# Kernel optimization log

Measured on AMD Instinct MI355X. Metric: run time of the kernel, lower is better.

Reference implementation:

```python
import jax, jax.numpy as jnp
import numpy as np

D_MODEL, KAN_HIDDEN, NUM, K = 1024, 128, 3, 3  # grid_size=3, spline order k=3
GRID_RANGE = (-1.0, 1.0)


def make_grid(in_dim):
    # extended grid: num+1 interior knots padded by k steps of h on each side -> num+1+2k points
    h = (GRID_RANGE[1] - GRID_RANGE[0]) / NUM
    g = jnp.arange(-K, NUM + K + 1, dtype=jnp.float32) * h + GRID_RANGE[0]  # [num+1+2k]
    return jnp.broadcast_to(g, (in_dim, g.shape[0]))  # [in_dim, G]


def b_splines(x, grid):
    # Cox-de-Boor recursion. x: [N, D], grid: [D, G] -> basis [N, D, G-1-K]
    xg = x[:, :, None]  # [N, D, 1]
    B = ((xg >= grid[None, :, :-1]) & (xg < grid[None, :, 1:])).astype(x.dtype)
    for d in range(1, K + 1):
        left = (xg - grid[None, :, : -(d + 1)]) / (grid[:, d:-1] - grid[:, : -(d + 1)])[None]
        right = (grid[None, :, d + 1:] - xg) / (grid[:, d + 1:] - grid[:, 1:-d])[None]
        B = left * B[:, :, :-1] + right * B[:, :, 1:]
    return B  # [N, D, NUM+K]


def kan_layer(x, grid, coef, scale_base, scale_sp):
    # y[n,i,o] = scale_base[i,o]*silu(x[n,i]) + scale_sp[i,o]*sum_g B[n,i,g]*coef[i,o,g]; out = y.sum(i)
    B = b_splines(x, grid)  # [N, in, NUM+K]
    spline = jnp.einsum('nig,iog->no', B, coef * scale_sp[:, :, None])
    base = jnp.einsum('ni,io->no', jax.nn.silu(x), scale_base)
    return base + spline  # [N, out]


def setup_inputs() -> dict:
    key = jax.random.key(0)
    ks = jax.random.split(key, 7)
    s = 0.1  # small init scale for spline coefficients, matching noisy init spirit
    return {
        'x': jax.random.normal(ks[0], (4, 4096, D_MODEL), dtype=jnp.float32),
        'coef1': jax.random.normal(ks[1], (D_MODEL, KAN_HIDDEN, NUM + K), dtype=jnp.float32) * s,
        'scale_base1': jax.random.normal(ks[2], (D_MODEL, KAN_HIDDEN), dtype=jnp.float32),
        'scale_sp1': jnp.ones((D_MODEL, KAN_HIDDEN), dtype=jnp.float32),
        'coef2': jax.random.normal(ks[3], (KAN_HIDDEN, D_MODEL, NUM + K), dtype=jnp.float32) * s,
        'scale_base2': jax.random.normal(ks[4], (KAN_HIDDEN, D_MODEL), dtype=jnp.float32),
        'scale_sp2': jnp.ones((KAN_HIDDEN, D_MODEL), dtype=jnp.float32),
    }


def reference(x, coef1, scale_base1, scale_sp1, coef2, scale_base2, scale_sp2):
    b, s, d = x.shape
    xf = x.reshape(-1, d)  # [N, d_model]
    g1 = make_grid(D_MODEL)
    g2 = make_grid(KAN_HIDDEN)
    y1 = kan_layer(xf, g1, coef1, scale_base1, scale_sp1)   # [N, kan_hidden]
    y2 = kan_layer(y1, g2, coef2, scale_base2, scale_sp2)   # [N, d_model]
    return y2.reshape(b, s, d)
```

## Files before the change

kernel.cpp:

```cpp
#include <hip/hip_runtime.h>
#include <stdint.h>

typedef float f32x4 __attribute__((ext_vector_type(4)));
typedef __bf16 bf16x8 __attribute__((ext_vector_type(8)));
typedef __bf16 bf16x2 __attribute__((ext_vector_type(2)));
typedef unsigned short ushort4v __attribute__((ext_vector_type(4)));

#define NROW 16384
#define DM   1024
#define HID  128
#define K1   8192
#define K2   1024
#define KSPLIT 4

__device__ __forceinline__ unsigned short f2bf(float f) {
  unsigned u = __builtin_bit_cast(unsigned, f);
  u += 0x7fffu + ((u >> 16) & 1u);
  return (unsigned short)(u >> 16);
}

__device__ __forceinline__ uint32_t pk2(float lo, float hi) {
  bf16x2 v;
  v[0] = (__bf16)lo;
  v[1] = (__bf16)hi;
  return __builtin_bit_cast(uint32_t, v);
}

__device__ __forceinline__ void g2l16(const void* g, void* l) {
  __builtin_amdgcn_global_load_lds(
      (const __attribute__((address_space(1))) unsigned int*)g,
      (__attribute__((address_space(3))) unsigned int*)l, 16, 0, 0);
}

__device__ __forceinline__ bf16x8 expand8(float v) {
  const float t = (v + 3.0f) * 1.5f;
  const float cf = floorf(t);
  const float u = t - cf;
  int c = (int)cf;
  c = c < -1 ? -1 : c;
  c = c > 9 ? 9 : c;
  const float u2 = u * u, u3 = u2 * u, omu = 1.0f - u;
  const float p0 = u3 * (1.0f / 6.0f);
  float p1 = __builtin_fmaf(0.5f, u, 1.0f / 6.0f);
  p1 = __builtin_fmaf(0.5f, u2, p1);
  p1 = __builtin_fmaf(-0.5f, u3, p1);
  float p2 = __builtin_fmaf(0.5f, u3, 4.0f / 6.0f);
  p2 = p2 - u2;
  const float p3 = (omu * omu) * (omu * (1.0f / 6.0f));
  const uint64_t W = (uint64_t)pk2(p3, p2) | ((uint64_t)pk2(p1, p0) << 32);
  const int sa = (c - 2) * 16;
  const int sl = sa & 63;
  const uint64_t t1 = W << sl;
  const uint64_t t2 = (W >> (63 - sl)) >> 1;
  const uint64_t t3 = W >> ((-sa) & 63);
  const uint64_t L = sa < 0 ? t3 : (sa < 64 ? t1 : 0);
  const uint64_t H = sa < 0 ? 0  : (sa < 64 ? t2 : t1);
  const float e = __expf(-v);
  const float s = v * __builtin_amdgcn_rcpf(1.0f + e);
  const uint32_t su = __builtin_bit_cast(uint32_t, s);
  const uint32_t shf_bits = su & 0xffff0000u;
  const float slo_f = s - __builtin_bit_cast(float, shf_bits);
  const uint32_t slo = (uint32_t)__builtin_bit_cast(unsigned short, (__bf16)slo_f);
  const uint32_t w0 = ((uint32_t)L & 0xffff0000u) | (shf_bits >> 16);
  const uint32_t w1 = (uint32_t)(L >> 32);
  const uint32_t w2 = (uint32_t)H;
  const uint32_t w3 = ((uint32_t)(H >> 32) & 0xffffu) | (slo << 16);
  union { uint4 q; bf16x8 b; } r;
  r.q = (uint4){w0, w1, w2, w3};
  return r.b;
}

__global__ void kan_prep_w1(const float* __restrict__ c1, const float* __restrict__ sb1,
                            const float* __restrict__ sp1, unsigned short* __restrict__ w1t) {
  const int t = blockIdx.x * 256 + threadIdx.x;
  const int o = t >> 10, i = t & 1023;
  const float sb = sb1[i * HID + o], sp = sp1[i * HID + o];
  const float* cf = c1 + (size_t)(i * HID + o) * 6;
  union { uint4 u; unsigned short h[8]; } r;
  const unsigned short b = f2bf(sb);
  r.h[0] = b; r.h[7] = b;
#pragma unroll
  for (int g = 0; g < 6; ++g) r.h[g + 1] = f2bf(cf[g] * sp);
  *(uint4*)(w1t + (size_t)o * K1 + i * 8) = r.u;
}

__global__ void kan_prep_w2(const float* __restrict__ c2, const float* __restrict__ sb2,
                            const float* __restrict__ sp2, unsigned short* __restrict__ w2t) {
  const int t = blockIdx.x * 256 + threadIdx.x;
  const int o = t >> 7, i = t & 127;
  const float sb = sb2[i * DM + o], sp = sp2[i * DM + o];
  const float* cf = c2 + (size_t)(i * DM + o) * 6;
  union { uint4 u; unsigned short h[8]; } r;
  const unsigned short b = f2bf(sb);
  r.h[0] = b; r.h[7] = b;
#pragma unroll
  for (int g = 0; g < 6; ++g) r.h[g + 1] = f2bf(cf[g] * sp);
  *(uint4*)(w2t + (size_t)o * K2 + i * 8) = r.u;
}

__global__ __launch_bounds__(256, 2) void kan_gemm1(
    const float* __restrict__ x, const unsigned short* __restrict__ w1t,
    unsigned short* __restrict__ yq) {
  __shared__ __align__(16) char lds[65536];
  const int tid = threadIdx.x;
  const int lane = tid & 63, w = tid >> 6;
  const int wm = w >> 1, wk = w & 1;
  const int mt = blockIdx.x >> 2, kh = blockIdx.x & 3;
  const int m0 = mt * 128;

  f32x4 acc[4][8];
#pragma unroll
  for (int a = 0; a < 4; ++a)
#pragma unroll
    for (int b = 0; b < 8; ++b) acc[a][b] = (f32x4){0.f, 0.f, 0.f, 0.f};

  const int arow = m0 + wm * 64 + (lane & 15);
  const float* xp[4];
#pragma unroll
  for (int mi = 0; mi < 4; ++mi)
    xp[mi] = x + (size_t)(arow + mi * 16) * DM + kh * 256 + wk * 4 + (lane >> 4);

  const unsigned short* bp =
      w1t + (size_t)(lane & 15) * K1 + kh * 2048 + wk * 32 + (lane >> 4) * 8;

  const int NT = 32;
  float xc[4], xn[4];
#pragma unroll
  for (int mi = 0; mi < 4; ++mi) xc[mi] = xp[mi][0];

  for (int kt = 0; kt < NT; ++kt) {
    bf16x8 b[8], af[4];
#pragma unroll
    for (int ni = 0; ni < 8; ++ni)
      b[ni] = *(const bf16x8*)(bp + (size_t)ni * 16 * K1 + kt * 64);
    const int nk = (kt + 1 < NT) ? kt + 1 : NT - 1;
#pragma unroll
    for (int mi = 0; mi < 4; ++mi) xn[mi] = xp[mi][nk * 8];
#pragma unroll
    for (int mi = 0; mi < 4; ++mi) af[mi] = expand8(xc[mi]);
#pragma unroll
    for (int mi = 0; mi < 4; ++mi)
#pragma unroll
      for (int ni = 0; ni < 8; ++ni)
        acc[mi][ni] = __builtin_amdgcn_mfma_f32_16x16x32_bf16(af[mi], b[ni], acc[mi][ni], 0, 0, 0);
#pragma unroll
    for (int mi = 0; mi < 4; ++mi) xc[mi] = xn[mi];
  }

  if (wk == 1) {
    char* r = lds + wm * 32768;
#pragma unroll
    for (int mi = 0; mi < 4; ++mi)
#pragma unroll
      for (int ni = 0; ni < 8; ++ni)
        *(f32x4*)(r + (mi * 8 + ni) * 1024 + lane * 16) = acc[mi][ni];
  }
  __syncthreads();
  if (wk == 0) {
    const char* r = lds + wm * 32768;
    unsigned short* yb = yq + (size_t)kh * NROW * HID;
#pragma unroll
    for (int mi = 0; mi < 4; ++mi)
#pragma unroll
      for (int ni = 0; ni < 8; ++ni) {
        f32x4 o = *(const f32x4*)(r + (mi * 8 + ni) * 1024 + lane * 16);
        o += acc[mi][ni];
        const int col = ni * 16 + (lane & 15);
#pragma unroll
        for (int rr = 0; rr < 4; ++rr) {
          const int row = wm * 64 + mi * 16 + (lane >> 4) * 4 + rr;
          yb[(size_t)(m0 + row) * HID + col] = __builtin_bit_cast(unsigned short, (__bf16)o[rr]);
        }
      }
  }
}

__global__ void kan_combine(const unsigned short* __restrict__ yq, unsigned short* __restrict__ a2) {
  const size_t i4 = ((size_t)blockIdx.x * 256 + threadIdx.x) * 4;
  float v[4] = {0.f, 0.f, 0.f, 0.f};
#pragma unroll
  for (int h = 0; h < KSPLIT; ++h) {
    ushort4v q = *(const ushort4v*)(yq + (size_t)h * NROW * HID + i4);
#pragma unroll
    for (int j = 0; j < 4; ++j)
      v[j] += __builtin_bit_cast(float, (uint32_t)q[j] << 16);
  }
#pragma unroll
  for (int j = 0; j < 4; ++j)
    *(bf16x8*)(a2 + (i4 + j) * 8) = expand8(v[j]);
}

__global__ __launch_bounds__(256, 2) void kan_gemm2(
    const unsigned short* __restrict__ a2, const unsigned short* __restrict__ w2t,
    float* __restrict__ out) {
  __shared__ __align__(16) unsigned short lds[2 * 16384];
  const int tid = threadIdx.x;
  const int lane = tid & 63, w = tid >> 6;
  const int wm = w >> 1, wn = w & 1;
  const int mt = blockIdx.x & 127, nt = blockIdx.x >> 7;
  const int m0 = mt * 128, n0 = nt * 128;

  f32x4 acc[4][4];
#pragma unroll
  for (int a = 0; a < 4; ++a)
#pragma unroll
    for (int b = 0; b < 4; ++b) acc[a][b] = (f32x4){0.f, 0.f, 0.f, 0.f};

  auto stage = [&](int kt, int buf) {
#pragma unroll
    for (int q = 0; q < 4; ++q) {
      const int r = (w * 4 + q) * 8 + (lane >> 3);
      const int slot = (lane & 7) ^ (lane >> 3);
      g2l16(a2 + (size_t)(m0 + r) * K2 + kt * 64 + slot * 8,
            (char*)lds + buf * 32768 + (w * 4 + q) * 1024);
      g2l16(w2t + (size_t)(n0 + r) * K2 + kt * 64 + slot * 8,
            (char*)lds + buf * 32768 + 16384 + (w * 4 + q) * 1024);
    }
  };

  stage(0, 0);
  for (int kt = 0; kt < 16; ++kt) {
    const int cur = kt & 1;
    if (kt + 1 < 16) {
      stage(kt + 1, cur ^ 1);
      asm volatile("s_waitcnt vmcnt(8)" ::: "memory");
    } else {
      asm volatile("s_waitcnt vmcnt(0)" ::: "memory");
    }
    __builtin_amdgcn_sched_barrier(0);
    __builtin_amdgcn_s_barrier();
    const char* ab = (const char*)lds + cur * 32768;
    const char* bb = ab + 16384;
#pragma unroll
    for (int ks = 0; ks < 2; ++ks) {
      bf16x8 af[4], bfr[4];
#pragma unroll
      for (int mi = 0; mi < 4; ++mi) {
        const int row = wm * 64 + mi * 16 + (lane & 15);
        af[mi] = *(const bf16x8*)(ab + ((row * 128 + ks * 64 + (lane >> 4) * 16) ^ ((row & 7) << 4)));
      }
#pragma unroll
      for (int ni = 0; ni < 4; ++ni) {
        const int col = wn * 64 + ni * 16 + (lane & 15);
        bfr[ni] = *(const bf16x8*)(bb + ((col * 128 + ks * 64 + (lane >> 4) * 16) ^ ((col & 7) << 4)));
      }
#pragma unroll
      for (int mi = 0; mi < 4; ++mi)
#pragma unroll
        for (int ni = 0; ni < 4; ++ni)
          acc[mi][ni] = __builtin_amdgcn_mfma_f32_16x16x32_bf16(af[mi], bfr[ni], acc[mi][ni], 0, 0, 0);
    }
    __builtin_amdgcn_s_barrier();
  }

#pragma unroll
  for (int mi = 0; mi < 4; ++mi)
#pragma unroll
    for (int r = 0; r < 4; ++r) {
      const int row = wm * 64 + mi * 16 + (lane >> 4) * 4 + r;
#pragma unroll
      for (int ni = 0; ni < 4; ++ni) {
        const int col = wn * 64 + ni * 16 + (lane & 15);
        out[(size_t)(m0 + row) * DM + n0 + col] = acc[mi][ni][r];
      }
    }
}

extern "C" void kernel_launch(void* const* d_in, const int* in_sizes, int n_in,
                              void* d_out, int out_size, void* d_ws, size_t ws_size,
                              hipStream_t stream) {
  const float* x   = (const float*)d_in[0];
  const float* c1  = (const float*)d_in[1];
  const float* sb1 = (const float*)d_in[2];
  const float* sp1 = (const float*)d_in[3];
  const float* c2  = (const float*)d_in[4];
  const float* sb2 = (const float*)d_in[5];
  const float* sp2 = (const float*)d_in[6];
  float* out = (float*)d_out;

  unsigned short* w1t = (unsigned short*)d_ws;
  unsigned short* w2t = w1t + (size_t)HID * K1;
  unsigned short* a2  = w2t + (size_t)DM * K2;
  unsigned short* yq  = a2 + (size_t)NROW * K2;

  kan_prep_w1<<<512, 256, 0, stream>>>(c1, sb1, sp1, w1t);
  kan_prep_w2<<<512, 256, 0, stream>>>(c2, sb2, sp2, w2t);
  kan_gemm1<<<512, 256, 0, stream>>>(x, w1t, yq);
  kan_combine<<<NROW * HID / 1024, 256, 0, stream>>>(yq, a2);
  kan_gemm2<<<(NROW / 128) * (DM / 128), 256, 0, stream>>>(a2, w2t, out);
}
```

Before: 157.5 us.

## Pre-swizzle layer-1 weights into MFMA fragment order and vectorize x loads

The layer-1 weight prep kernel now writes bf16 weights in a packed layout that matches the MFMA fragment order per wave, so each lane's B loads are contiguous across the wave instead of strided by K1 rows. The k-assignment of x is changed so each lane reads four consecutive floats with one 16-byte load per four k-steps, rather than one scalar load per step. This targets uncoalesced global loads in gemm1. It also changes which input features each wave and lane cover, which must stay consistent with the new weight layout.

```diff
diff --git a/kernel.cpp b/kernel.cpp
--- a/kernel.cpp
+++ b/kernel.cpp
@@ -71,7 +71,7 @@
 }
 
 __global__ void kan_prep_w1(const float* __restrict__ c1, const float* __restrict__ sb1,
-                            const float* __restrict__ sp1, unsigned short* __restrict__ w1t) {
+                            const float* __restrict__ sp1, unsigned short* __restrict__ w1p) {
   const int t = blockIdx.x * 256 + threadIdx.x;
   const int o = t >> 10, i = t & 1023;
   const float sb = sb1[i * HID + o], sp = sp1[i * HID + o];
@@ -81,7 +81,11 @@
   r.h[0] = b; r.h[7] = b;
 #pragma unroll
   for (int g = 0; g < 6; ++g) r.h[g + 1] = f2bf(cf[g] * sp);
-  *(uint4*)(w1t + (size_t)o * K1 + i * 8) = r.u;
+  const int kh = i >> 8, iq = i & 255;
+  const int wk = iq >> 7, gg = (iq >> 5) & 3, it = iq & 31;
+  const int lane = gg * 16 + (o & 15), ni = o >> 4;
+  const size_t flat = (size_t)kh * 262144 + it * 8192 + wk * 4096 + ni * 512 + lane * 8;
+  *(uint4*)(w1p + flat) = r.u;
 }
 
 __global__ void kan_prep_w2(const float* __restrict__ c2, const float* __restrict__ sb2,
@@ -99,7 +103,7 @@
 }
 
 __global__ __launch_bounds__(256, 2) void kan_gemm1(
-    const float* __restrict__ x, const unsigned short* __restrict__ w1t,
+    const float* __restrict__ x, const unsigned short* __restrict__ w1p,
     unsigned short* __restrict__ yq) {
   __shared__ __align__(16) char lds[65536];
   const int tid = threadIdx.x;
@@ -107,6 +111,7 @@
   const int wm = w >> 1, wk = w & 1;
   const int mt = blockIdx.x >> 2, kh = blockIdx.x & 3;
   const int m0 = mt * 128;
+  const int g = lane >> 4;
 
   f32x4 acc[4][8];
 #pragma unroll
@@ -118,33 +123,36 @@
   const float* xp[4];
 #pragma unroll
   for (int mi = 0; mi < 4; ++mi)
-    xp[mi] = x + (size_t)(arow + mi * 16) * DM + kh * 256 + wk * 4 + (lane >> 4);
-
-  const unsigned short* bp =
-      w1t + (size_t)(lane & 15) * K1 + kh * 2048 + wk * 32 + (lane >> 4) * 8;
-
-  const int NT = 32;
-  float xc[4], xn[4];
-#pragma unroll
-  for (int mi = 0; mi < 4; ++mi) xc[mi] = xp[mi][0];
-
-  for (int kt = 0; kt < NT; ++kt) {
-    bf16x8 b[8], af[4];
-#pragma unroll
-    for (int ni = 0; ni < 8; ++ni)
-      b[ni] = *(const bf16x8*)(bp + (size_t)ni * 16 * K1 + kt * 64);
-    const int nk = (kt + 1 < NT) ? kt + 1 : NT - 1;
-#pragma unroll
-    for (int mi = 0; mi < 4; ++mi) xn[mi] = xp[mi][nk * 8];
-#pragma unroll
-    for (int mi = 0; mi < 4; ++mi) af[mi] = expand8(xc[mi]);
-#pragma unroll
-    for (int mi = 0; mi < 4; ++mi)
+    xp[mi] = x + (size_t)(arow + mi * 16) * DM + kh * 256 + wk * 128 + g * 32;
+
+  const unsigned short* bp = w1p + (size_t)kh * 262144 + wk * 4096 + lane * 8;
+
+  f32x4 xq[4], xn[4];
+#pragma unroll
+  for (int mi = 0; mi < 4; ++mi) xq[mi] = *(const f32x4*)(xp[mi]);
+
+  for (int c4 = 0; c4 < 8; ++c4) {
+    if (c4 + 1 < 8) {
+#pragma unroll
+      for (int mi = 0; mi < 4; ++mi) xn[mi] = *(const f32x4*)(xp[mi] + (c4 + 1) * 4);
+    }
+#pragma unroll
+    for (int it4 = 0; it4 < 4; ++it4) {
+      const int it = c4 * 4 + it4;
+      bf16x8 b[8], af[4];
 #pragma unroll
       for (int ni = 0; ni < 8; ++ni)
-        acc[mi][ni] = __builtin_amdgcn_mfma_f32_16x16x32_bf16(af[mi], b[ni], acc[mi][ni], 0, 0, 0);
-#pragma unroll
-    for (int mi = 0; mi < 4; ++mi) xc[mi] = xn[mi];
+        b[ni] = *(const bf16x8*)(bp + (size_t)it * 8192 + ni * 512);
+#pragma unroll
+      for (int mi = 0; mi < 4; ++mi) af[mi] = expand8(xq[mi][it4]);
+#pragma unroll
+      for (int mi = 0; mi < 4; ++mi)
+#pragma unroll
+        for (int ni = 0; ni < 8; ++ni)
+          acc[mi][ni] = __builtin_amdgcn_mfma_f32_16x16x32_bf16(af[mi], b[ni], acc[mi][ni], 0, 0, 0);
+    }
+#pragma unroll
+    for (int mi = 0; mi < 4; ++mi) xq[mi] = xn[mi];
   }
 
   if (wk == 1) {
@@ -278,14 +286,14 @@
   const float* sp2 = (const float*)d_in[6];
   float* out = (float*)d_out;
 
-  unsigned short* w1t = (unsigned short*)d_ws;
-  unsigned short* w2t = w1t + (size_t)HID * K1;
+  unsigned short* w1p = (unsigned short*)d_ws;
+  unsigned short* w2t = w1p + (size_t)HID * K1;
   unsigned short* a2  = w2t + (size_t)DM * K2;
   unsigned short* yq  = a2 + (size_t)NROW * K2;
 
-  kan_prep_w1<<<512, 256, 0, stream>>>(c1, sb1, sp1, w1t);
+  kan_prep_w1<<<512, 256, 0, stream>>>(c1, sb1, sp1, w1p);
   kan_prep_w2<<<512, 256, 0, stream>>>(c2, sb2, sp2, w2t);
-  kan_gemm1<<<512, 256, 0, stream>>>(x, w1t, yq);
+  kan_gemm1<<<512, 256, 0, stream>>>(x, w1p, yq);
   kan_combine<<<NROW * HID / 1024, 256, 0, stream>>>(yq, a2);
   kan_gemm2<<<(NROW / 128) * (DM / 128), 256, 0, stream>>>(a2, w2t, out);
 }
```

Measured after the change: 151.8 us. -3.6%, faster.
